# Kernel tuning notes

Hardware: AMD Instinct MI355X
Metric: run time of the kernel (lower is better)

Reference implementation:

```python
import jax, jax.numpy as jnp
import numpy as np

B, N, L, E, R = 16384, 1024, 3, 8, 64


def _xavier(key, shape):
    # torch xavier_normal_ on (E, a, b): fan_in=b, fan_out=a (last two dims)
    fan_in, fan_out = shape[-1], shape[-2]
    std = float(np.sqrt(2.0 / (fan_in + fan_out)))
    return jax.random.normal(key, shape, dtype=jnp.float32) * std


def setup_inputs() -> dict:
    key = jax.random.key(0)
    ks = jax.random.split(key, 6)
    x = jax.random.normal(ks[0], (B, N), dtype=jnp.float32)
    U = _xavier(ks[1], (L, E, N, R))   # U_kernels per layer
    V = _xavier(ks[2], (L, E, R, N))   # V_kernels per layer
    C = _xavier(ks[3], (L, E, R, R))   # C_kernels per layer
    bias = jnp.zeros((L, N), dtype=jnp.float32)
    # gate Linear(N, 1, bias=False) per expert; torch default init kaiming_uniform
    bound = float(1.0 / np.sqrt(N))
    gate_w = jax.random.uniform(ks[4], (E, N), dtype=jnp.float32,
                                minval=-bound, maxval=bound)
    return {"x": x, "U": U, "V": V, "C": C, "bias": bias, "gate_w": gate_w}


def reference(x, U, V, C, bias, gate_w):
    x0 = x                                     # [B, N]
    x_l = x0
    for l in range(L):
        # gating logits per expert: [B, E], softmax over experts
        gates = jax.nn.softmax(jnp.einsum('bn,en->be', x_l, gate_w), axis=1)
        # low-rank expert chain, vectorized over experts
        v = jnp.einsum('ern,bn->ber', V[l], x_l)            # [B, E, R]
        c = jnp.einsum('ers,bes->ber', C[l], jax.nn.relu(v))  # [B, E, R]
        u = jnp.einsum('enr,ber->ben', U[l], jax.nn.relu(c))  # [B, E, N]
        experts = x0[:, None, :] * (u + bias[l][None, None, :])  # [B, E, N]
        moe = jnp.einsum('ben,be->bn', experts, gates)        # [B, N]
        x_l = moe + x_l
    return x_l
```

## Files before the change

### kernel.cpp

```cpp
#include <hip/hip_runtime.h>
#include <hip/hip_bf16.h>
#include <stdint.h>
#include <stddef.h>

typedef __bf16 bf16;
typedef __bf16 bf16x4 __attribute__((ext_vector_type(4)));
typedef __bf16 bf16x8 __attribute__((ext_vector_type(8)));
typedef float f32x4 __attribute__((ext_vector_type(4)));

#define BROWS 16384
#define NDIM 1024
#define NLAYERS 3

__device__ __forceinline__ void gld_lds16(const bf16* g, bf16* l) {
    __builtin_amdgcn_global_load_lds(
        (const __attribute__((address_space(1))) void*)g,
        (__attribute__((address_space(3))) void*)l, 16, 0, 0);
}

__global__ __launch_bounds__(256) void cvt_bf16_kernel(
    const float* __restrict__ src, bf16* __restrict__ dst, int n4)
{
    int i = blockIdx.x * 256 + threadIdx.x;
    if (i < n4) {
        float4 v = ((const float4*)src)[i];
        bf16x4 b;
        b[0] = (bf16)v.x; b[1] = (bf16)v.y; b[2] = (bf16)v.z; b[3] = (bf16)v.w;
        ((bf16x4*)dst)[i] = b;
    }
}

__global__ __launch_bounds__(256) void wu_transpose_kernel(
    const float* __restrict__ U, bf16* __restrict__ wu)
{
    int d = blockIdx.x * 256 + threadIdx.x;
    int r = d & 63;
    int e = (d >> 6) & 7;
    int n = (d >> 9) & 1023;
    int l = d >> 19;
    size_t s = (((size_t)(l * 8 + e)) * 1024 + n) * 64 + r;
    wu[d] = (bf16)U[s];
}

__global__ __launch_bounds__(256) void gwp_kernel(
    const float* __restrict__ gw, bf16* __restrict__ gwp)
{
    int d = (blockIdx.x * 256 + threadIdx.x) * 4;
    int k  = d & 63;
    int e  = (d >> 6) & 15;
    int kt = d >> 10;
    bf16x4 b = {};
    if (e < 8) {
        float4 v = *(const float4*)&gw[e * 1024 + kt * 64 + k];
        b[0] = (bf16)v.x; b[1] = (bf16)v.y; b[2] = (bf16)v.z; b[3] = (bf16)v.w;
    }
    *(bf16x4*)&gwp[d] = b;
}

template<int KDIM>
__global__ __launch_bounds__(256) void gemm_vc_kernel(
    const bf16* __restrict__ A, const bf16* __restrict__ Bt,
    const float* __restrict__ Cwl, const bf16* __restrict__ gwp,
    bf16* __restrict__ cp)
{
    __shared__ __align__(16) bf16 smem[27648];
    bf16* As = smem;
    bf16* Bs = smem + 8192;
    bf16* Cs = smem + 16384;
    bf16* Gs = smem + 24576;
    float* g_lds = (float*)(smem + 25600);

    const int tid = threadIdx.x;
    const int wv = tid >> 6, ln = tid & 63;
    const long bm = (long)blockIdx.y * 128;
    const long bn = (long)blockIdx.x * 128;
    const int wm = (wv >> 1) << 6, wn = (wv & 1) << 6;
    const int e_loc = wv & 1;
    f32x4 acc[4][4] = {};
    f32x4 accg[4] = {};

    {
        const float* Cg = Cwl + (size_t)(blockIdx.x * 2) * 4096;
#pragma unroll
        for (int i = 0; i < 8; ++i) {
            int f = tid * 32 + i * 4;
            float4 cv = *(const float4*)&Cg[f];
            int ee = f >> 12;
            int r  = (f >> 6) & 63;
            int s  = f & 63;
            bf16x4 b;
            b[0] = (bf16)cv.x; b[1] = (bf16)cv.y; b[2] = (bf16)cv.z; b[3] = (bf16)cv.w;
            char* base = (char*)Cs + ee * 8192;
            *(bf16x4*)(base + ((r * 128 + s * 2) ^ ((r & 7) << 4))) = b;
        }
    }

    const int srow = tid >> 3;
    const int scol = (tid & 7) * 8;
    const bf16* Abase = A + (bm + srow) * (long)KDIM + scol;
    const bf16* Bbase = Bt + (bn + srow) * (long)KDIM + scol;
    bf16* Asl = &As[(tid & ~63) * 8];
    bf16* Bsl = &Bs[(tid & ~63) * 8];

    for (int kt = 0; kt < KDIM / 64; ++kt) {
        const int k0 = kt * 64;
        __syncthreads();
#pragma unroll
        for (int t = 0; t < 4; ++t) {
            gld_lds16(Abase + (long)t * 32 * KDIM + k0, Asl + t * 2048);
            gld_lds16(Bbase + (long)t * 32 * KDIM + k0, Bsl + t * 2048);
        }
        if (wv == 3) {
            gld_lds16(gwp + kt * 1024 + ln * 8, Gs);
            gld_lds16(gwp + kt * 1024 + 512 + ln * 8, Gs + 512);
        }
        __syncthreads();
#pragma unroll
        for (int kc = 0; kc < 2; ++kc) {
            bf16x8 af[4], bfr[4];
#pragma unroll
            for (int i = 0; i < 4; ++i) {
                af[i]  = *(const bf16x8*)&As[(wm + i * 16 + (ln & 15)) * 64 + kc * 32 + (ln >> 4) * 8];
                bfr[i] = *(const bf16x8*)&Bs[(wn + i * 16 + (ln & 15)) * 64 + kc * 32 + (ln >> 4) * 8];
            }
#pragma unroll
            for (int mi = 0; mi < 4; ++mi)
#pragma unroll
                for (int ni = 0; ni < 4; ++ni)
                    acc[mi][ni] = __builtin_amdgcn_mfma_f32_16x16x32_bf16(
                        af[mi], bfr[ni], acc[mi][ni], 0, 0, 0);
            if ((wv & 1) == 0) {
                bf16x8 gfr = *(const bf16x8*)&Gs[(ln & 15) * 64 + kc * 32 + (ln >> 4) * 8];
#pragma unroll
                for (int mi = 0; mi < 4; ++mi)
                    accg[mi] = __builtin_amdgcn_mfma_f32_16x16x32_bf16(
                        af[mi], gfr, accg[mi], 0, 0, 0);
            }
        }
    }

    __syncthreads();

    const int cr = (ln >> 4) * 4, cc = ln & 15;

    if ((wv & 1) == 0) {
#pragma unroll
        for (int mi = 0; mi < 4; ++mi)
#pragma unroll
            for (int j = 0; j < 4; ++j) {
                float l = accg[mi][j];
                float m = l;
#pragma unroll
                for (int msk = 1; msk <= 4; msk <<= 1)
                    m = fmaxf(m, __shfl_xor(l, msk));
                float m2 = l;
                m2 = fmaxf(m2, __shfl_xor(m2, 1));
                m2 = fmaxf(m2, __shfl_xor(m2, 2));
                m2 = fmaxf(m2, __shfl_xor(m2, 4));
                float ex = __expf(l - m2);
                float s = ex;
                s += __shfl_xor(s, 1);
                s += __shfl_xor(s, 2);
                s += __shfl_xor(s, 4);
                if (cc < 8) {
                    int row = wm + mi * 16 + cr + j;
                    g_lds[row * 8 + cc] = ex / s;
                }
            }
    }

    char* vsb = (char*)smem + wv * 8192;
#pragma unroll
    for (int mi = 0; mi < 4; ++mi)
#pragma unroll
        for (int ni = 0; ni < 4; ++ni)
#pragma unroll
            for (int j = 0; j < 4; ++j) {
                int row = mi * 16 + cr + j;
                int col = ni * 16 + cc;
                *(bf16*)(vsb + ((row * 128 + col * 2) ^ ((row & 7) << 4))) =
                    (bf16)fmaxf(acc[mi][ni][j], 0.f);
            }
    __syncthreads();

    f32x4 acc2[4][4] = {};
    char* csb = (char*)Cs + e_loc * 8192;
#pragma unroll
    for (int kc = 0; kc < 2; ++kc) {
        bf16x8 af[4], bfr[4];
        const int sb = (kc * 32 + (ln >> 4) * 8) * 2;
#pragma unroll
        for (int i = 0; i < 4; ++i) {
            int ra = i * 16 + (ln & 15);
            af[i]  = *(const bf16x8*)(vsb + ((ra * 128 + sb) ^ ((ra & 7) << 4)));
            bfr[i] = *(const bf16x8*)(csb + ((ra * 128 + sb) ^ ((ra & 7) << 4)));
        }
#pragma unroll
        for (int mi = 0; mi < 4; ++mi)
#pragma unroll
            for (int ni = 0; ni < 4; ++ni)
                acc2[mi][ni] = __builtin_amdgcn_mfma_f32_16x16x32_bf16(
                    af[mi], bfr[ni], acc2[mi][ni], 0, 0, 0);
    }

    const int e_g = (int)(blockIdx.x * 2) + e_loc;
#pragma unroll
    for (int mi = 0; mi < 4; ++mi)
#pragma unroll
        for (int j = 0; j < 4; ++j) {
            int wrow = wm + mi * 16 + cr + j;
            long row = bm + wrow;
            float g = g_lds[wrow * 8 + e_g];
#pragma unroll
            for (int ni = 0; ni < 4; ++ni) {
                long col = bn + wn + ni * 16 + cc;
                cp[row * 512 + col] = (bf16)(fmaxf(acc2[mi][ni][j], 0.f) * g);
            }
        }
}

template<bool XL_IS_X0, bool WRITE_XB>
__global__ __launch_bounds__(256) void gemm2_kernel(
    const bf16* __restrict__ A, const bf16* __restrict__ Bt,
    const float* __restrict__ xl, const bf16* __restrict__ xb0,
    const float* __restrict__ bias, float* __restrict__ out,
    bf16* __restrict__ xbn)
{
    __shared__ __align__(16) bf16 As[128 * 64];
    __shared__ __align__(16) bf16 Bs[64 * 64];
    const int tid = threadIdx.x;
    const int wv = tid >> 6, ln = tid & 63;
    const long bm = (long)blockIdx.y * 128;
    const long bn = (long)blockIdx.x * 64;
    const int wm = (wv >> 1) << 6, wn = (wv & 1) << 5;
    f32x4 acc[4][2] = {};

    const int srow = tid >> 3;
    const int scol = (tid & 7) * 8;
    const bf16* Abase = A + (bm + srow) * 512L + scol;
    const bf16* Bbase = Bt + (bn + srow) * 512L + scol;
    bf16* Asl = &As[(tid & ~63) * 8];
    bf16* Bsl = &Bs[(tid & ~63) * 8];

    for (int kt = 0; kt < 8; ++kt) {
        const int k0 = kt * 64;
        __syncthreads();
#pragma unroll
        for (int t = 0; t < 4; ++t)
            gld_lds16(Abase + (long)t * 32 * 512 + k0, Asl + t * 2048);
#pragma unroll
        for (int t = 0; t < 2; ++t)
            gld_lds16(Bbase + (long)t * 32 * 512 + k0, Bsl + t * 2048);
        __syncthreads();
#pragma unroll
        for (int kc = 0; kc < 2; ++kc) {
            bf16x8 af[4], bfr[2];
#pragma unroll
            for (int i = 0; i < 4; ++i)
                af[i]  = *(const bf16x8*)&As[(wm + i * 16 + (ln & 15)) * 64 + kc * 32 + (ln >> 4) * 8];
#pragma unroll
            for (int i = 0; i < 2; ++i)
                bfr[i] = *(const bf16x8*)&Bs[(wn + i * 16 + (ln & 15)) * 64 + kc * 32 + (ln >> 4) * 8];
#pragma unroll
            for (int mi = 0; mi < 4; ++mi)
#pragma unroll
                for (int ni = 0; ni < 2; ++ni)
                    acc[mi][ni] = __builtin_amdgcn_mfma_f32_16x16x32_bf16(
                        af[mi], bfr[ni], acc[mi][ni], 0, 0, 0);
        }
    }

    const int cr = (ln >> 4) * 4, cc = ln & 15;
#pragma unroll
    for (int mi = 0; mi < 4; ++mi)
#pragma unroll
        for (int ni = 0; ni < 2; ++ni) {
            long col = bn + wn + ni * 16 + cc;
            float bcol = bias[col];
#pragma unroll
            for (int j = 0; j < 4; ++j) {
                long row = bm + wm + mi * 16 + cr + j;
                long idx = row * 1024L + col;
                float xlv = xl[idx];
                float mul = XL_IS_X0 ? xlv : (float)xb0[idx];
                float o = xlv + mul * (acc[mi][ni][j] + bcol);
                out[idx] = o;
                if (WRITE_XB) xbn[idx] = (bf16)o;
            }
        }
}

extern "C" void kernel_launch(void* const* d_in, const int* in_sizes, int n_in,
                              void* d_out, int out_size, void* d_ws, size_t ws_size,
                              hipStream_t stream)
{
    const float* x0   = (const float*)d_in[0];
    const float* U    = (const float*)d_in[1];
    const float* V    = (const float*)d_in[2];
    const float* Cw   = (const float*)d_in[3];
    const float* bias = (const float*)d_in[4];
    const float* gw   = (const float*)d_in[5];
    float* out = (float*)d_out;

    char* ws = (char*)d_ws;
    bf16*  wvw  = (bf16*)ws;
    bf16*  wu   = (bf16*)(ws + 3145728);
    bf16*  gwp  = (bf16*)(ws + 6291456);
    bf16*  xb0  = (bf16*)(ws + 6324224);
    bf16*  xbn  = (bf16*)(ws + 6324224 + 33554432);
    bf16*  cp   = (bf16*)(ws + 6324224 + 2 * 33554432);

    cvt_bf16_kernel<<<1536, 256, 0, stream>>>(V, wvw, 393216);
    cvt_bf16_kernel<<<16384, 256, 0, stream>>>(x0, xb0, 4194304);
    wu_transpose_kernel<<<6144, 256, 0, stream>>>(U, wu);
    gwp_kernel<<<16, 256, 0, stream>>>(gw, gwp);

    for (int l = 0; l < NLAYERS; ++l) {
        const bf16* xbl = (l == 0) ? xb0 : xbn;
        const float* xl = (l == 0) ? x0 : out;
        gemm_vc_kernel<1024><<<dim3(4, 128), 256, 0, stream>>>(
            xbl, wvw + (size_t)l * 524288, Cw + (size_t)l * 32768, gwp, cp);
        const bf16* wul = wu + (size_t)l * 524288;
        const float* bl = bias + (size_t)l * 1024;
        if (l == 0)
            gemm2_kernel<true, true><<<dim3(16, 128), 256, 0, stream>>>(
                cp, wul, xl, nullptr, bl, out, xbn);
        else if (l == 1)
            gemm2_kernel<false, true><<<dim3(16, 128), 256, 0, stream>>>(
                cp, wul, xl, xb0, bl, out, xbn);
        else
            gemm2_kernel<false, false><<<dim3(16, 128), 256, 0, stream>>>(
                cp, wul, xl, xb0, bl, out, nullptr);
    }
}
```

Baseline: 422.3 us.

## Keep residual stream in bf16, widen gemm2 tiles, read gate weights directly

The residual state between layers is now held only in bf16 and updated in place. Intermediate layers no longer read or write the fp32 output; only the last layer writes fp32. The gemm2 tile grows from 128x64 to 128x128, halving the grid and reducing re-reads of the cp operand. The gating MFMA work is split across all four waves, with the gate fragment loaded straight from global memory instead of staged in LDS, and the first kernel gets a 3-blocks-per-CU occupancy hint. This cuts fp32 memory traffic at the cost of extra rounding error, since the residual is accumulated in bf16.

Measured after the change: 995.5 us. +135.7%, slower.

```diff
diff --git a/kernel.cpp b/kernel.cpp
--- a/kernel.cpp
+++ b/kernel.cpp
@@ -58,17 +58,16 @@
 }
 
 template<int KDIM>
-__global__ __launch_bounds__(256) void gemm_vc_kernel(
+__global__ __launch_bounds__(256, 3) void gemm_vc_kernel(
     const bf16* __restrict__ A, const bf16* __restrict__ Bt,
     const float* __restrict__ Cwl, const bf16* __restrict__ gwp,
     bf16* __restrict__ cp)
 {
-    __shared__ __align__(16) bf16 smem[27648];
+    __shared__ __align__(16) bf16 smem[26624];
     bf16* As = smem;
     bf16* Bs = smem + 8192;
     bf16* Cs = smem + 16384;
-    bf16* Gs = smem + 24576;
-    float* g_lds = (float*)(smem + 25600);
+    float* g_lds = (float*)(smem + 24576);
 
     const int tid = threadIdx.x;
     const int wv = tid >> 6, ln = tid & 63;
@@ -76,8 +75,9 @@
     const long bn = (long)blockIdx.x * 128;
     const int wm = (wv >> 1) << 6, wn = (wv & 1) << 6;
     const int e_loc = wv & 1;
+    const int gm = (wv & 1) * 2;
     f32x4 acc[4][4] = {};
-    f32x4 accg[4] = {};
+    f32x4 accg[2] = {};
 
     {
         const float* Cg = Cwl + (size_t)(blockIdx.x * 2) * 4096;
@@ -110,10 +110,6 @@
             gld_lds16(Abase + (long)t * 32 * KDIM + k0, Asl + t * 2048);
             gld_lds16(Bbase + (long)t * 32 * KDIM + k0, Bsl + t * 2048);
         }
-        if (wv == 3) {
-            gld_lds16(gwp + kt * 1024 + ln * 8, Gs);
-            gld_lds16(gwp + kt * 1024 + 512 + ln * 8, Gs + 512);
-        }
         __syncthreads();
 #pragma unroll
         for (int kc = 0; kc < 2; ++kc) {
@@ -123,19 +119,17 @@
                 af[i]  = *(const bf16x8*)&As[(wm + i * 16 + (ln & 15)) * 64 + kc * 32 + (ln >> 4) * 8];
                 bfr[i] = *(const bf16x8*)&Bs[(wn + i * 16 + (ln & 15)) * 64 + kc * 32 + (ln >> 4) * 8];
             }
+            bf16x8 gfr = *(const bf16x8*)&gwp[kt * 1024 + (ln & 15) * 64 + kc * 32 + (ln >> 4) * 8];
 #pragma unroll
             for (int mi = 0; mi < 4; ++mi)
 #pragma unroll
                 for (int ni = 0; ni < 4; ++ni)
                     acc[mi][ni] = __builtin_amdgcn_mfma_f32_16x16x32_bf16(
                         af[mi], bfr[ni], acc[mi][ni], 0, 0, 0);
-            if ((wv & 1) == 0) {
-                bf16x8 gfr = *(const bf16x8*)&Gs[(ln & 15) * 64 + kc * 32 + (ln >> 4) * 8];
-#pragma unroll
-                for (int mi = 0; mi < 4; ++mi)
-                    accg[mi] = __builtin_amdgcn_mfma_f32_16x16x32_bf16(
-                        af[mi], gfr, accg[mi], 0, 0, 0);
-            }
+#pragma unroll
+            for (int q = 0; q < 2; ++q)
+                accg[q] = __builtin_amdgcn_mfma_f32_16x16x32_bf16(
+                    af[gm + q], gfr, accg[q], 0, 0, 0);
         }
     }
 
@@ -143,31 +137,25 @@
 
     const int cr = (ln >> 4) * 4, cc = ln & 15;
 
-    if ((wv & 1) == 0) {
-#pragma unroll
-        for (int mi = 0; mi < 4; ++mi)
-#pragma unroll
-            for (int j = 0; j < 4; ++j) {
-                float l = accg[mi][j];
-                float m = l;
-#pragma unroll
-                for (int msk = 1; msk <= 4; msk <<= 1)
-                    m = fmaxf(m, __shfl_xor(l, msk));
-                float m2 = l;
-                m2 = fmaxf(m2, __shfl_xor(m2, 1));
-                m2 = fmaxf(m2, __shfl_xor(m2, 2));
-                m2 = fmaxf(m2, __shfl_xor(m2, 4));
-                float ex = __expf(l - m2);
-                float s = ex;
-                s += __shfl_xor(s, 1);
-                s += __shfl_xor(s, 2);
-                s += __shfl_xor(s, 4);
-                if (cc < 8) {
-                    int row = wm + mi * 16 + cr + j;
-                    g_lds[row * 8 + cc] = ex / s;
-                }
-            }
-    }
+#pragma unroll
+    for (int q = 0; q < 2; ++q)
+#pragma unroll
+        for (int j = 0; j < 4; ++j) {
+            float lg = accg[q][j];
+            float m2 = lg;
+            m2 = fmaxf(m2, __shfl_xor(m2, 1));
+            m2 = fmaxf(m2, __shfl_xor(m2, 2));
+            m2 = fmaxf(m2, __shfl_xor(m2, 4));
+            float ex = __expf(lg - m2);
+            float s = ex;
+            s += __shfl_xor(s, 1);
+            s += __shfl_xor(s, 2);
+            s += __shfl_xor(s, 4);
+            if (cc < 8) {
+                int row = wm + (gm + q) * 16 + cr + j;
+                g_lds[row * 8 + cc] = ex / s;
+            }
+        }
 
     char* vsb = (char*)smem + wv * 8192;
 #pragma unroll
@@ -219,21 +207,21 @@
         }
 }
 
-template<bool XL_IS_X0, bool WRITE_XB>
+template<bool BASE_IS_MUL, bool WRITE_F32>
 __global__ __launch_bounds__(256) void gemm2_kernel(
     const bf16* __restrict__ A, const bf16* __restrict__ Bt,
-    const float* __restrict__ xl, const bf16* __restrict__ xb0,
+    const bf16* __restrict__ xbl, const bf16* __restrict__ xb0,
     const float* __restrict__ bias, float* __restrict__ out,
     bf16* __restrict__ xbn)
 {
     __shared__ __align__(16) bf16 As[128 * 64];
-    __shared__ __align__(16) bf16 Bs[64 * 64];
+    __shared__ __align__(16) bf16 Bs[128 * 64];
     const int tid = threadIdx.x;
     const int wv = tid >> 6, ln = tid & 63;
     const long bm = (long)blockIdx.y * 128;
-    const long bn = (long)blockIdx.x * 64;
-    const int wm = (wv >> 1) << 6, wn = (wv & 1) << 5;
-    f32x4 acc[4][2] = {};
+    const long bn = (long)blockIdx.x * 128;
+    const int wm = (wv >> 1) << 6, wn = (wv & 1) << 6;
+    f32x4 acc[4][4] = {};
 
     const int srow = tid >> 3;
     const int scol = (tid & 7) * 8;
@@ -246,25 +234,23 @@
         const int k0 = kt * 64;
         __syncthreads();
 #pragma unroll
-        for (int t = 0; t < 4; ++t)
+        for (int t = 0; t < 4; ++t) {
             gld_lds16(Abase + (long)t * 32 * 512 + k0, Asl + t * 2048);
-#pragma unroll
-        for (int t = 0; t < 2; ++t)
             gld_lds16(Bbase + (long)t * 32 * 512 + k0, Bsl + t * 2048);
+        }
         __syncthreads();
 #pragma unroll
         for (int kc = 0; kc < 2; ++kc) {
-            bf16x8 af[4], bfr[2];
-#pragma unroll
-            for (int i = 0; i < 4; ++i)
+            bf16x8 af[4], bfr[4];
+#pragma unroll
+            for (int i = 0; i < 4; ++i) {
                 af[i]  = *(const bf16x8*)&As[(wm + i * 16 + (ln & 15)) * 64 + kc * 32 + (ln >> 4) * 8];
-#pragma unroll
-            for (int i = 0; i < 2; ++i)
                 bfr[i] = *(const bf16x8*)&Bs[(wn + i * 16 + (ln & 15)) * 64 + kc * 32 + (ln >> 4) * 8];
+            }
 #pragma unroll
             for (int mi = 0; mi < 4; ++mi)
 #pragma unroll
-                for (int ni = 0; ni < 2; ++ni)
+                for (int ni = 0; ni < 4; ++ni)
                     acc[mi][ni] = __builtin_amdgcn_mfma_f32_16x16x32_bf16(
                         af[mi], bfr[ni], acc[mi][ni], 0, 0, 0);
         }
@@ -274,18 +260,18 @@
 #pragma unroll
     for (int mi = 0; mi < 4; ++mi)
 #pragma unroll
-        for (int ni = 0; ni < 2; ++ni) {
+        for (int ni = 0; ni < 4; ++ni) {
             long col = bn + wn + ni * 16 + cc;
             float bcol = bias[col];
 #pragma unroll
             for (int j = 0; j < 4; ++j) {
                 long row = bm + wm + mi * 16 + cr + j;
                 long idx = row * 1024L + col;
-                float xlv = xl[idx];
-                float mul = XL_IS_X0 ? xlv : (float)xb0[idx];
-                float o = xlv + mul * (acc[mi][ni][j] + bcol);
-                out[idx] = o;
-                if (WRITE_XB) xbn[idx] = (bf16)o;
+                float mul = (float)xb0[idx];
+                float base = BASE_IS_MUL ? mul : (float)xbl[idx];
+                float o = base + mul * (acc[mi][ni][j] + bcol);
+                if (WRITE_F32) out[idx] = o;
+                else           xbn[idx] = (bf16)o;
             }
         }
 }
@@ -307,7 +293,7 @@
     bf16*  wu   = (bf16*)(ws + 3145728);
     bf16*  gwp  = (bf16*)(ws + 6291456);
     bf16*  xb0  = (bf16*)(ws + 6324224);
-    bf16*  xbn  = (bf16*)(ws + 6324224 + 33554432);
+    bf16*  xba  = (bf16*)(ws + 6324224 + 33554432);
     bf16*  cp   = (bf16*)(ws + 6324224 + 2 * 33554432);
 
     cvt_bf16_kernel<<<1536, 256, 0, stream>>>(V, wvw, 393216);
@@ -316,20 +302,19 @@
     gwp_kernel<<<16, 256, 0, stream>>>(gw, gwp);
 
     for (int l = 0; l < NLAYERS; ++l) {
-        const bf16* xbl = (l == 0) ? xb0 : xbn;
-        const float* xl = (l == 0) ? x0 : out;
+        const bf16* xbl = (l == 0) ? xb0 : xba;
         gemm_vc_kernel<1024><<<dim3(4, 128), 256, 0, stream>>>(
             xbl, wvw + (size_t)l * 524288, Cw + (size_t)l * 32768, gwp, cp);
         const bf16* wul = wu + (size_t)l * 524288;
         const float* bl = bias + (size_t)l * 1024;
         if (l == 0)
-            gemm2_kernel<true, true><<<dim3(16, 128), 256, 0, stream>>>(
-                cp, wul, xl, nullptr, bl, out, xbn);
+            gemm2_kernel<true, false><<<dim3(8, 128), 256, 0, stream>>>(
+                cp, wul, nullptr, xb0, bl, nullptr, xba);
         else if (l == 1)
-            gemm2_kernel<false, true><<<dim3(16, 128), 256, 0, stream>>>(
-                cp, wul, xl, xb0, bl, out, xbn);
+            gemm2_kernel<false, false><<<dim3(8, 128), 256, 0, stream>>>(
+                cp, wul, xba, xb0, bl, nullptr, xba);
         else
-            gemm2_kernel<false, false><<<dim3(16, 128), 256, 0, stream>>>(
-                cp, wul, xl, xb0, bl, out, nullptr);
-    }
-}
+            gemm2_kernel<false, true><<<dim3(8, 128), 256, 0, stream>>>(
+                cp, wul, xba, xb0, bl, out, nullptr);
+    }
+}
```
